# Kernel tuning notes

Hardware: AMD Instinct MI355X
Metric: run time of the kernel (lower is better)

Reference implementation:

```python
import jax, jax.numpy as jnp
import numpy as np

B, N, F = 32, 1024, 32
EPS = 1e-5


def _bn(h):
    # torch BatchNorm1d(x.size(1)) applied to [B, N, C]: normalizes each node index
    # over (batch, channel) axes, training mode, biased variance, weight=1, bias=0.
    m = h.mean(axis=(0, 2), keepdims=True)
    v = h.var(axis=(0, 2), keepdims=True)
    return (h - m) / jnp.sqrt(v + EPS)


def setup_inputs() -> dict:
    key = jax.random.key(0)
    ks = jax.random.split(key, 16)
    x = jax.random.normal(ks[0], (B, N, F), dtype=jnp.float32)
    adj = jax.random.uniform(ks[1], (B, N, N), dtype=jnp.float32)

    def w(k, i, o):
        return jax.random.normal(k, (i, o), dtype=jnp.float32) * (1.0 / np.sqrt(i))

    inp = {
        'x': x, 'adj': adj,
        'W1': w(ks[2], F, 4), 'b1': jnp.zeros((4,), jnp.float32),
        'W2': w(ks[3], 4, 2), 'b2': jnp.zeros((2,), jnp.float32),
        'W3': w(ks[4], 6, 4), 'b3': jnp.zeros((4,), jnp.float32),
        'W5': w(ks[5], 6, 4), 'b5': jnp.zeros((4,), jnp.float32),
        'W7': w(ks[6], 6, 4), 'b7': jnp.zeros((4,), jnp.float32),
        'Wl': w(ks[7], 24, 3), 'bl': jnp.zeros((3,), jnp.float32),
    }
    return inp


def reference(x, adj, W1, b1, W2, b2, W3, b3, W5, b5, W7, b7, Wl, bl):
    n = adj.shape[-1]
    # DenseGCNConv normalization (identical for every conv call): set diag to 1,
    # then D^{-1/2} A D^{-1/2} with degree clamped at 1. Precompute once.
    diag = jnp.eye(n, dtype=bool)
    A = jnp.where(diag, jnp.asarray(1.0, adj.dtype), adj)  # [B,N,N]
    d = jnp.clip(A.sum(-1), 1.0, None) ** -0.5              # [B,N]
    A = d[:, :, None] * A * d[:, None, :]

    def gcn(h, W, b):
        return jnp.matmul(A, jnp.matmul(h, W)) + b

    def block(h, Wa, ba):
        x1 = _bn(jax.nn.relu(gcn(h, Wa, ba)))      # [B,N,4]
        x2 = _bn(jax.nn.relu(gcn(x1, W2, b2)))     # [B,N,2] (conv2 reused)
        x12 = jnp.concatenate([x1, x2], axis=-1)   # [B,N,6]
        return x12, x12.max(axis=1)                # pooled [B,6]

    h, p1 = block(x, W1, b1)
    h, p2 = block(h, W3, b3)
    h, p3 = block(h, W5, b5)
    h, p4 = block(h, W7, b7)
    out = jnp.concatenate([p1, p2, p3, p4], axis=-1)  # [B,24]
    ypred = out @ Wl + bl                             # [B,3]
    return ypred
```

## Files before the change

### kernel.cpp

```cpp
#include <hip/hip_runtime.h>
#include <hip/hip_fp16.h>

#define NB 32
#define NN 1024

typedef _Float16 h2 __attribute__((ext_vector_type(2)));
typedef _Float16 h8 __attribute__((ext_vector_type(8)));

static const size_t F_D     = 0;
static const size_t F_STATS = 32768;
static const size_t F_XW1   = 49152;
static constexpr size_t F_Y[8] = {180224, 311296, 376832, 507904,
                                  573440, 704512, 770048, 901120};
static const size_t AH_BYTE_OFF  = 3866624;
static const size_t WS_NEED_HALF = AH_BYTE_OFF + (size_t)NB*NN*NN*2;

__device__ __forceinline__ float fdot2f(h2 a, h2 b, float c) {
#if __has_builtin(__builtin_amdgcn_fdot2)
    return __builtin_amdgcn_fdot2(a, b, c, false);
#else
    return c + (float)a[0]*(float)b[0] + (float)a[1]*(float)b[1];
#endif
}

__global__ __launch_bounds__(256)
void k0_prep(const float* __restrict__ adj, const float* __restrict__ x,
             const float* __restrict__ W1, float* __restrict__ dd,
             float* __restrict__ xw1, float* __restrict__ stats,
             __half* __restrict__ ahw)
{
    const int tid = threadIdx.x;
    const int bx  = blockIdx.x;
    if (bx < 8192) {
        const int lane = tid & 63, wid = tid >> 6;
        const int row = bx * 4 + wid;
        const int n = row & (NN - 1);
        const float4* arow = (const float4*)(adj + (size_t)row * NN);
        uint2* hrow = (uint2*)(ahw + (size_t)row * NN);
        float s = 0.f;
        #pragma unroll
        for (int it = 0; it < 4; ++it) {
            const int idx = lane + it * 64;
            float4 v = arow[idx];
            const int k0 = idx * 4;
            v.x = (k0 + 0 == n) ? 1.f : v.x;
            v.y = (k0 + 1 == n) ? 1.f : v.y;
            v.z = (k0 + 2 == n) ? 1.f : v.z;
            v.w = (k0 + 3 == n) ? 1.f : v.w;
            s += v.x + v.y + v.z + v.w;
            if (ahw) {
                __half2 h01 = __floats2half2_rn(v.x, v.y);
                __half2 h23 = __floats2half2_rn(v.z, v.w);
                uint2 u;
                u.x = *(unsigned*)&h01; u.y = *(unsigned*)&h23;
                hrow[idx] = u;
            }
        }
        #pragma unroll
        for (int m = 1; m < 64; m <<= 1) s += __shfl_xor(s, m);
        if (lane == 0) dd[row] = rsqrtf(fmaxf(s, 1.f));
    } else if (bx < 8320) {
        const int id = (bx - 8192) * 256 + tid;
        const float4* xr = (const float4*)(x + (size_t)id * 32);
        float in[32];
        #pragma unroll
        for (int i = 0; i < 8; ++i) {
            float4 v = xr[i];
            in[4*i]=v.x; in[4*i+1]=v.y; in[4*i+2]=v.z; in[4*i+3]=v.w;
        }
        float o[4] = {0.f,0.f,0.f,0.f};
        #pragma unroll
        for (int i = 0; i < 32; ++i)
            #pragma unroll
            for (int c = 0; c < 4; ++c) o[c] += in[i] * W1[i*4+c];
        *(float4*)(xw1 + (size_t)id * 4) = make_float4(o[0],o[1],o[2],o[3]);
    } else {
        const int id = (bx - 8320) * 256 + tid;
        stats[id] = 0.f;
    }
}

template<int CIN1, int CIN2, int COUT>
__global__ __launch_bounds__(512, 4)
void pass_half(const __half* __restrict__ ah, const float* __restrict__ dd,
               const float* __restrict__ xw1,
               const float* __restrict__ src1, const float* __restrict__ st1,
               const float* __restrict__ src2, const float* __restrict__ st2,
               const float* __restrict__ W, const float* __restrict__ bias,
               float* __restrict__ Y, float* __restrict__ stout)
{
    constexpr int HG = 8*COUT + 4;
    __shared__ _Float16 XPt[128 * HG];
    const int tid = threadIdx.x, lane = tid & 63, wid = tid >> 6;
    const int g = lane >> 5, l32 = lane & 31;
    const int b = blockIdx.x >> 4;
    const int tile = (blockIdx.x & 15) << 6;

    for (int k = tid; k < NN; k += 512) {
        float xw[COUT];
        if constexpr (CIN1 == 0) {
            const float4 v = *(const float4*)(xw1 + ((size_t)b*NN + k) * 4);
            xw[0]=v.x; xw[1]=v.y; xw[2]=v.z; xw[3]=v.w;
        } else {
            float in[CIN1 + CIN2];
            {
                const float cnt = 1.f / (32.f * CIN1);
                const float m  = st1[k] * cnt;
                const float ms = st1[NN + k] * cnt;
                const float iv = rsqrtf(ms - m*m + 1e-5f);
                const float4 v = *(const float4*)(src1 + ((size_t)b*NN + k) * CIN1);
                in[0]=(v.x-m)*iv; in[1]=(v.y-m)*iv; in[2]=(v.z-m)*iv; in[3]=(v.w-m)*iv;
            }
            if constexpr (CIN2 > 0) {
                const float cnt = 1.f / (32.f * CIN2);
                const float m  = st2[k] * cnt;
                const float ms = st2[NN + k] * cnt;
                const float iv = rsqrtf(ms - m*m + 1e-5f);
                const float2 v = *(const float2*)(src2 + ((size_t)b*NN + k) * CIN2);
                in[CIN1+0]=(v.x-m)*iv; in[CIN1+1]=(v.y-m)*iv;
            }
            #pragma unroll
            for (int c = 0; c < COUT; ++c) {
                float s = 0.f;
                #pragma unroll
                for (int i = 0; i < CIN1+CIN2; ++i) s += in[i]*W[i*COUT+c];
                xw[c] = s;
            }
        }
        const float dk = dd[b*NN + k];
        const int mbase = (k>>3)*HG + ((k>>1)&3)*(2*COUT) + (k&1);
        #pragma unroll
        for (int c = 0; c < COUT; ++c)
            XPt[mbase + 2*c] = (_Float16)(xw[c]*dk);
    }
    __syncthreads();

    const int r0 = tile + wid*8 + g*4;
    const __half* ab[4];
    #pragma unroll
    for (int j = 0; j < 4; ++j)
        ab[j] = ah + ((size_t)(b*NN + r0 + j)) * NN;

    float acc[4][COUT];
    #pragma unroll
    for (int j = 0; j < 4; ++j)
        #pragma unroll
        for (int c = 0; c < COUT; ++c) acc[j][c] = 0.f;

    #pragma unroll
    for (int it = 0; it < 4; ++it) {
        const int k = it*256 + l32*8;
        h8 av[4];
        #pragma unroll
        for (int j = 0; j < 4; ++j) av[j] = *(const h8*)(ab[j] + k);
        const h8* xp = (const h8*)&XPt[(k>>3) * HG];
        h8 xt[COUT];
        #pragma unroll
        for (int q = 0; q < COUT; ++q) xt[q] = xp[q];
        const h2* x2 = (const h2*)&xt[0];
        #pragma unroll
        for (int j = 0; j < 4; ++j) {
            const h2* a2 = (const h2*)&av[j];
            #pragma unroll
            for (int c = 0; c < COUT; ++c) {
                float s = acc[j][c];
                #pragma unroll
                for (int p = 0; p < 4; ++p)
                    s = fdot2f(a2[p], x2[p*COUT + c], s);
                acc[j][c] = s;
            }
        }
    }

    #pragma unroll
    for (int j = 0; j < 4; ++j)
        #pragma unroll
        for (int c = 0; c < COUT; ++c) {
            float v = acc[j][c];
            v += __shfl_xor(v, 1);  v += __shfl_xor(v, 2);
            v += __shfl_xor(v, 4);  v += __shfl_xor(v, 8);
            v += __shfl_xor(v, 16);
            acc[j][c] = v;
        }
    if (l32 == 0) {
        #pragma unroll
        for (int j = 0; j < 4; ++j) {
            const int n = r0 + j;
            const float dn = dd[b*NN + n];
            float s = 0.f, q2 = 0.f;
            float y[COUT];
            #pragma unroll
            for (int c = 0; c < COUT; ++c) {
                float t = acc[j][c] * dn + bias[c];
                t = fmaxf(t, 0.f);
                y[c] = t; s += t; q2 += t*t;
            }
            if constexpr (COUT == 4)
                *(float4*)(Y + ((size_t)(b*NN + n))*4) = make_float4(y[0],y[1],y[2],y[3]);
            else
                *(float2*)(Y + ((size_t)(b*NN + n))*2) = make_float2(y[0],y[1]);
            atomicAdd(stout + n, s);
            atomicAdd(stout + NN + n, q2);
        }
    }
}

template<int CIN1, int CIN2, int COUT>
__global__ __launch_bounds__(512)
void pass_f32(const float* __restrict__ adj, const float* __restrict__ dd,
              const float* __restrict__ xw1,
              const float* __restrict__ src1, const float* __restrict__ st1,
              const float* __restrict__ src2, const float* __restrict__ st2,
              const float* __restrict__ W, const float* __restrict__ bias,
              float* __restrict__ Y, float* __restrict__ stout)
{
    __shared__ float XP[COUT][NN + (NN/32)*4];
    const int tid  = threadIdx.x;
    const int b    = blockIdx.x >> 5;
    const int tile = (blockIdx.x & 31) * 32;

    for (int k = tid; k < NN; k += 512) {
        float xw[COUT];
        if constexpr (CIN1 == 0) {
            const float4 v = *(const float4*)(xw1 + ((size_t)b*NN + k) * 4);
            xw[0]=v.x; xw[1]=v.y; xw[2]=v.z; xw[3]=v.w;
        } else {
            float in[CIN1 + CIN2];
            {
                const float cnt = 1.f / (32.f * CIN1);
                float m  = st1[k] * cnt;
                float ms = st1[NN + k] * cnt;
                float iv = rsqrtf(ms - m*m + 1e-5f);
                const float4 v = *(const float4*)(src1 + ((size_t)b*NN + k) * CIN1);
                in[0]=(v.x-m)*iv; in[1]=(v.y-m)*iv; in[2]=(v.z-m)*iv; in[3]=(v.w-m)*iv;
            }
            if constexpr (CIN2 > 0) {
                const float cnt = 1.f / (32.f * CIN2);
                float m  = st2[k] * cnt;
                float ms = st2[NN + k] * cnt;
                float iv = rsqrtf(ms - m*m + 1e-5f);
                const float2 v = *(const float2*)(src2 + ((size_t)b*NN + k) * CIN2);
                in[CIN1+0]=(v.x-m)*iv; in[CIN1+1]=(v.y-m)*iv;
            }
            #pragma unroll
            for (int c = 0; c < COUT; ++c) {
                float s = 0.f;
                #pragma unroll
                for (int i = 0; i < CIN1+CIN2; ++i) s += in[i]*W[i*COUT+c];
                xw[c] = s;
            }
        }
        const float dk = dd[(size_t)b*NN + k];
        const int mk = k + ((k >> 5) << 2);
        #pragma unroll
        for (int c = 0; c < COUT; ++c) XP[c][mk] = xw[c]*dk;
    }
    __syncthreads();

    const int lane = tid & 63, wid = tid >> 6;
    const int r0 = tile + wid * 4;
    float acc[4][COUT];
    #pragma unroll
    for (int j = 0; j < 4; ++j)
        #pragma unroll
        for (int c = 0; c < COUT; ++c) acc[j][c] = 0.f;
    float dn[4]; size_t rb[4];
    #pragma unroll
    for (int j = 0; j < 4; ++j) {
        dn[j] = dd[(size_t)b*NN + r0 + j];
        rb[j] = ((size_t)(b*NN + r0 + j)) * NN;
    }
    #pragma unroll
    for (int it = 0; it < 4; ++it) {
        const int kw = 4 * (lane + 64 * it);
        const int mb = kw + ((kw >> 5) << 2);
        float xwv[COUT][4];
        #pragma unroll
        for (int c = 0; c < COUT; ++c) {
            const float4 v = *(const float4*)&XP[c][mb];
            xwv[c][0]=v.x; xwv[c][1]=v.y; xwv[c][2]=v.z; xwv[c][3]=v.w;
        }
        #pragma unroll
        for (int j = 0; j < 4; ++j) {
            const int rr = r0 + j;
            float4 a = *(const float4*)(adj + rb[j] + kw);
            a.x = (kw + 0 == rr) ? 1.f : a.x;
            a.y = (kw + 1 == rr) ? 1.f : a.y;
            a.z = (kw + 2 == rr) ? 1.f : a.z;
            a.w = (kw + 3 == rr) ? 1.f : a.w;
            #pragma unroll
            for (int c = 0; c < COUT; ++c) {
                float s = acc[j][c];
                s = fmaf(a.x, xwv[c][0], s); s = fmaf(a.y, xwv[c][1], s);
                s = fmaf(a.z, xwv[c][2], s); s = fmaf(a.w, xwv[c][3], s);
                acc[j][c] = s;
            }
        }
    }
    #pragma unroll
    for (int j = 0; j < 4; ++j) {
        #pragma unroll
        for (int c = 0; c < COUT; ++c) {
            float v = acc[j][c];
            #pragma unroll
            for (int m = 1; m < 64; m <<= 1) v += __shfl_xor(v, m);
            acc[j][c] = v;
        }
        if (lane == 0) {
            float s = 0.f, q = 0.f;
            #pragma unroll
            for (int c = 0; c < COUT; ++c) {
                float y = acc[j][c] * dn[j] + bias[c];
                y = fmaxf(y, 0.f);
                Y[((size_t)(b*NN + r0 + j)) * COUT + c] = y;
                s += y; q += y * y;
            }
            atomicAdd(stout + (r0 + j), s);
            atomicAdd(stout + NN + (r0 + j), q);
        }
    }
}

__global__ __launch_bounds__(256)
void k_final(const float* __restrict__ Y1, const float* __restrict__ Y2,
             const float* __restrict__ Y3, const float* __restrict__ Y4,
             const float* __restrict__ Y5, const float* __restrict__ Y6,
             const float* __restrict__ Y7, const float* __restrict__ Y8,
             const float* __restrict__ stats,
             const float* __restrict__ Wl, const float* __restrict__ bl,
             float* __restrict__ out)
{
    const float* Ya[4] = {Y1, Y3, Y5, Y7};
    const float* Yb[4] = {Y2, Y4, Y6, Y8};
    const int b = blockIdx.x, tid = threadIdx.x;
    float mx[24];
    #pragma unroll
    for (int i = 0; i < 24; ++i) mx[i] = -3.4e38f;

    for (int n = tid; n < NN; n += 256) {
        #pragma unroll
        for (int g = 0; g < 4; ++g) {
            {
                const float* st = stats + (size_t)(2*g) * 2048;
                const float cnt = 1.f / 128.f;
                float m  = st[n] * cnt;
                float ms = st[NN + n] * cnt;
                float iv = rsqrtf(ms - m*m + 1e-5f);
                const float4 v = *(const float4*)(Ya[g] + ((size_t)b*NN + n) * 4);
                mx[g*6+0] = fmaxf(mx[g*6+0], (v.x - m) * iv);
                mx[g*6+1] = fmaxf(mx[g*6+1], (v.y - m) * iv);
                mx[g*6+2] = fmaxf(mx[g*6+2], (v.z - m) * iv);
                mx[g*6+3] = fmaxf(mx[g*6+3], (v.w - m) * iv);
            }
            {
                const float* st = stats + (size_t)(2*g+1) * 2048;
                const float cnt = 1.f / 64.f;
                float m  = st[n] * cnt;
                float ms = st[NN + n] * cnt;
                float iv = rsqrtf(ms - m*m + 1e-5f);
                const float2 v = *(const float2*)(Yb[g] + ((size_t)b*NN + n) * 2);
                mx[g*6+4] = fmaxf(mx[g*6+4], (v.x - m) * iv);
                mx[g*6+5] = fmaxf(mx[g*6+5], (v.y - m) * iv);
            }
        }
    }
    const int lane = tid & 63, wid = tid >> 6;
    #pragma unroll
    for (int i = 0; i < 24; ++i) {
        float v = mx[i];
        #pragma unroll
        for (int m = 1; m < 64; m <<= 1) v = fmaxf(v, __shfl_xor(v, m));
        mx[i] = v;
    }
    __shared__ float red[4][24];
    __shared__ float pooled[24];
    if (lane == 0) {
        #pragma unroll
        for (int i = 0; i < 24; ++i) red[wid][i] = mx[i];
    }
    __syncthreads();
    if (tid < 24)
        pooled[tid] = fmaxf(fmaxf(red[0][tid], red[1][tid]),
                            fmaxf(red[2][tid], red[3][tid]));
    __syncthreads();
    if (tid < 3) {
        float s = bl[tid];
        #pragma unroll
        for (int c = 0; c < 24; ++c) s += pooled[c] * Wl[c*3 + tid];
        out[b*3 + tid] = s;
    }
}

extern "C" void kernel_launch(void* const* d_in, const int* in_sizes, int n_in,
                              void* d_out, int out_size, void* d_ws, size_t ws_size,
                              hipStream_t stream)
{
    const float* x   = (const float*)d_in[0];
    const float* adj = (const float*)d_in[1];
    const float* W1  = (const float*)d_in[2];
    const float* b1  = (const float*)d_in[3];
    const float* W2  = (const float*)d_in[4];
    const float* b2  = (const float*)d_in[5];
    const float* W3  = (const float*)d_in[6];
    const float* b3  = (const float*)d_in[7];
    const float* W5  = (const float*)d_in[8];
    const float* b5  = (const float*)d_in[9];
    const float* W7  = (const float*)d_in[10];
    const float* b7  = (const float*)d_in[11];
    const float* Wl  = (const float*)d_in[12];
    const float* bl  = (const float*)d_in[13];
    float* out = (float*)d_out;

    float* wsf   = (float*)d_ws;
    float* dd    = wsf + F_D;
    float* stats = wsf + F_STATS;
    float* xw1   = wsf + F_XW1;
    float* Y[8];
    #pragma unroll
    for (int i = 0; i < 8; ++i) Y[i] = wsf + F_Y[i];
    __half* ah = (__half*)((char*)d_ws + AH_BYTE_OFF);
    const bool use_half = (ws_size >= WS_NEED_HALF);

    k0_prep<<<8384, 256, 0, stream>>>(adj, x, W1, dd, xw1, stats,
                                      use_half ? ah : nullptr);

    #define STT(i) (stats + (i)*2048)
    if (use_half) {
        const dim3 pg(512), pb(512);
        pass_half<0,0,4><<<pg, pb, 0, stream>>>(ah, dd, xw1,
            nullptr, nullptr, nullptr, nullptr, nullptr, b1, Y[0], STT(0));
        pass_half<4,0,2><<<pg, pb, 0, stream>>>(ah, dd, nullptr,
            Y[0], STT(0), nullptr, nullptr, W2, b2, Y[1], STT(1));
        pass_half<4,2,4><<<pg, pb, 0, stream>>>(ah, dd, nullptr,
            Y[0], STT(0), Y[1], STT(1), W3, b3, Y[2], STT(2));
        pass_half<4,0,2><<<pg, pb, 0, stream>>>(ah, dd, nullptr,
            Y[2], STT(2), nullptr, nullptr, W2, b2, Y[3], STT(3));
        pass_half<4,2,4><<<pg, pb, 0, stream>>>(ah, dd, nullptr,
            Y[2], STT(2), Y[3], STT(3), W5, b5, Y[4], STT(4));
        pass_half<4,0,2><<<pg, pb, 0, stream>>>(ah, dd, nullptr,
            Y[4], STT(4), nullptr, nullptr, W2, b2, Y[5], STT(5));
        pass_half<4,2,4><<<pg, pb, 0, stream>>>(ah, dd, nullptr,
            Y[4], STT(4), Y[5], STT(5), W7, b7, Y[6], STT(6));
        pass_half<4,0,2><<<pg, pb, 0, stream>>>(ah, dd, nullptr,
            Y[6], STT(6), nullptr, nullptr, W2, b2, Y[7], STT(7));
    } else {
        const dim3 pg(1024), pb(512);
        pass_f32<0,0,4><<<pg, pb, 0, stream>>>(adj, dd, xw1,
            nullptr, nullptr, nullptr, nullptr, nullptr, b1, Y[0], STT(0));
        pass_f32<4,0,2><<<pg, pb, 0, stream>>>(adj, dd, nullptr,
            Y[0], STT(0), nullptr, nullptr, W2, b2, Y[1], STT(1));
        pass_f32<4,2,4><<<pg, pb, 0, stream>>>(adj, dd, nullptr,
            Y[0], STT(0), Y[1], STT(1), W3, b3, Y[2], STT(2));
        pass_f32<4,0,2><<<pg, pb, 0, stream>>>(adj, dd, nullptr,
            Y[2], STT(2), nullptr, nullptr, W2, b2, Y[3], STT(3));
        pass_f32<4,2,4><<<pg, pb, 0, stream>>>(adj, dd, nullptr,
            Y[2], STT(2), Y[3], STT(3), W5, b5, Y[4], STT(4));
        pass_f32<4,0,2><<<pg, pb, 0, stream>>>(adj, dd, nullptr,
            Y[4], STT(4), nullptr, nullptr, W2, b2, Y[5], STT(5));
        pass_f32<4,2,4><<<pg, pb, 0, stream>>>(adj, dd, nullptr,
            Y[4], STT(4), Y[5], STT(5), W7, b7, Y[6], STT(6));
        pass_f32<4,0,2><<<pg, pb, 0, stream>>>(adj, dd, nullptr,
            Y[6], STT(6), nullptr, nullptr, W2, b2, Y[7], STT(7));
    }
    #undef STT

    k_final<<<32, 256, 0, stream>>>(Y[0], Y[1], Y[2], Y[3], Y[4], Y[5], Y[6], Y[7],
                                    stats, Wl, bl, out);
}
```

Before: 182.0 us.

## Double-buffer adjacency tiles into LDS via async global_load_lds with XOR swizzle

Stages the fp16 adjacency row tile for each 256-column chunk into a double-buffered shared-memory region using direct global-to-LDS loads, so the next chunk's fetch overlaps the current chunk's dot products. The first chunk is issued before the X*W preprocessing to hide its latency, and an XOR swizzle on columns is meant to avoid LDS bank conflicts. This adds 64KB of LDS per block, which likely lowers occupancy below the launch-bounds target, and adds barriers each chunk.

```diff
diff --git a/kernel.cpp b/kernel.cpp
--- a/kernel.cpp
+++ b/kernel.cpp
@@ -80,6 +80,28 @@
     }
 }
 
+__device__ __forceinline__ void stage_chunk(const __half* __restrict__ ah,
+        int rowbase, int wid, int lane, int ck, char* sbuf)
+{
+    #pragma unroll
+    for (int i = 0; i < 4; ++i) {
+        const int ob = (wid << 12) + (i << 10);
+        const int o  = ob + (lane << 4);
+        const int row = o >> 9;
+        const int scol = (o & 511) ^ ((row & 7) << 4);
+        const char* g = (const char*)ah +
+            (((size_t)(rowbase + row)) * NN + (size_t)ck * 256) * 2 + scol;
+#if __has_builtin(__builtin_amdgcn_global_load_lds)
+        __builtin_amdgcn_global_load_lds(
+            (const __attribute__((address_space(1))) void*)g,
+            (__attribute__((address_space(3))) void*)(sbuf + ob),
+            16, 0, 0);
+#else
+        *(float4*)(sbuf + o) = *(const float4*)g;
+#endif
+    }
+}
+
 template<int CIN1, int CIN2, int COUT>
 __global__ __launch_bounds__(512, 4)
 void pass_half(const __half* __restrict__ ah, const float* __restrict__ dd,
@@ -89,12 +111,16 @@
                const float* __restrict__ W, const float* __restrict__ bias,
                float* __restrict__ Y, float* __restrict__ stout)
 {
-    constexpr int HG = 8*COUT + 4;
+    constexpr int HG = (COUT == 4) ? 40 : 24;
+    __shared__ char sA[2][32768];
     __shared__ _Float16 XPt[128 * HG];
     const int tid = threadIdx.x, lane = tid & 63, wid = tid >> 6;
     const int g = lane >> 5, l32 = lane & 31;
     const int b = blockIdx.x >> 4;
     const int tile = (blockIdx.x & 15) << 6;
+    const int rowbase = b * NN + tile;
+
+    stage_chunk(ah, rowbase, wid, lane, 0, sA[0]);
 
     for (int k = tid; k < NN; k += 512) {
         float xw[COUT];
@@ -133,34 +159,35 @@
         for (int c = 0; c < COUT; ++c)
             XPt[mbase + 2*c] = (_Float16)(xw[c]*dk);
     }
+    asm volatile("s_waitcnt vmcnt(0)" ::: "memory");
     __syncthreads();
 
-    const int r0 = tile + wid*8 + g*4;
-    const __half* ab[4];
+    const int tr0 = wid*8 + g*4;
+    float acc[4][COUT];
     #pragma unroll
     for (int j = 0; j < 4; ++j)
-        ab[j] = ah + ((size_t)(b*NN + r0 + j)) * NN;
-
-    float acc[4][COUT];
-    #pragma unroll
-    for (int j = 0; j < 4; ++j)
         #pragma unroll
         for (int c = 0; c < COUT; ++c) acc[j][c] = 0.f;
 
-    #pragma unroll
-    for (int it = 0; it < 4; ++it) {
-        const int k = it*256 + l32*8;
-        h8 av[4];
-        #pragma unroll
-        for (int j = 0; j < 4; ++j) av[j] = *(const h8*)(ab[j] + k);
-        const h8* xp = (const h8*)&XPt[(k>>3) * HG];
+    int buf = 0;
+    for (int ck = 0; ck < 4; ++ck) {
+        if (ck < 3) stage_chunk(ah, rowbase, wid, lane, ck+1, sA[buf^1]);
+
+        const int g_i = ck*32 + l32;
         h8 xt[COUT];
-        #pragma unroll
-        for (int q = 0; q < COUT; ++q) xt[q] = xp[q];
+        {
+            const h8* xp = (const h8*)&XPt[g_i * HG];
+            #pragma unroll
+            for (int q = 0; q < COUT; ++q) xt[q] = xp[q];
+        }
         const h2* x2 = (const h2*)&xt[0];
+
         #pragma unroll
         for (int j = 0; j < 4; ++j) {
-            const h2* a2 = (const h2*)&av[j];
+            const int tr = tr0 + j;
+            const h8 av = *(const h8*)(&sA[buf][(tr << 9) +
+                                      ((l32 ^ (tr & 7)) << 4)]);
+            const h2* a2 = (const h2*)&av;
             #pragma unroll
             for (int c = 0; c < COUT; ++c) {
                 float s = acc[j][c];
@@ -170,6 +197,9 @@
                 acc[j][c] = s;
             }
         }
+        asm volatile("s_waitcnt vmcnt(0)" ::: "memory");
+        __syncthreads();
+        buf ^= 1;
     }
 
     #pragma unroll
@@ -185,7 +215,7 @@
     if (l32 == 0) {
         #pragma unroll
         for (int j = 0; j < 4; ++j) {
-            const int n = r0 + j;
+            const int n = tile + tr0 + j;
             const float dn = dd[b*NN + n];
             float s = 0.f, q2 = 0.f;
             float y[COUT];
```

Measured after the change: 206.2 us. +13.3%, slower.

## Stage adjacency tiles into LDS via async global_load_lds overlapping XW compute

Applied to the files above, without the earlier changes.

Each block now handles 32 rows instead of 64 and issues asynchronous global-to-LDS loads (global_load_lds) for its 64KB slab of the half-precision adjacency before computing the scaled XW vector. This lets the adjacency fetch overlap the preamble work. The XW operand layout changes to a channel-major array, the wave reduction now spans 64 lanes, and the grid doubles while occupancy bounds drop to 2 blocks per CU. The cost is heavier LDS use (64KB plus XW per block), lower occupancy, and the preamble being recomputed twice as often across blocks. There is also some risk in the hand-written vmcnt waits and the fallback path.

```diff
diff --git a/kernel.cpp b/kernel.cpp
--- a/kernel.cpp
+++ b/kernel.cpp
@@ -80,8 +80,27 @@
     }
 }
 
+__device__ __forceinline__ void stage_chunk32(const __half* __restrict__ ah,
+        int rowbase, int wid, int lane, int ck, char* sbase)
+{
+    #pragma unroll
+    for (int i = 0; i < 4; ++i) {
+        char* dst = sbase + (ck << 15) + (wid << 12) + (i << 10);
+        const char* g = (const char*)ah +
+            (((size_t)(rowbase + (wid << 2) + i)) << 11) + (ck << 10) + (lane << 4);
+#if __has_builtin(__builtin_amdgcn_global_load_lds)
+        __builtin_amdgcn_global_load_lds(
+            (const __attribute__((address_space(1))) void*)g,
+            (__attribute__((address_space(3))) void*)dst,
+            16, 0, 0);
+#else
+        *(float4*)(dst + lane * 16) = *(const float4*)g;
+#endif
+    }
+}
+
 template<int CIN1, int CIN2, int COUT>
-__global__ __launch_bounds__(512, 4)
+__global__ __launch_bounds__(512, 2)
 void pass_half(const __half* __restrict__ ah, const float* __restrict__ dd,
                const float* __restrict__ xw1,
                const float* __restrict__ src1, const float* __restrict__ st1,
@@ -89,14 +108,19 @@
                const float* __restrict__ W, const float* __restrict__ bias,
                float* __restrict__ Y, float* __restrict__ stout)
 {
-    constexpr int HG = 8*COUT + 4;
-    __shared__ _Float16 XPt[128 * HG];
+    __shared__ char sA[65536];
+    __shared__ _Float16 XPc[COUT][NN];
     const int tid = threadIdx.x, lane = tid & 63, wid = tid >> 6;
-    const int g = lane >> 5, l32 = lane & 31;
-    const int b = blockIdx.x >> 4;
-    const int tile = (blockIdx.x & 15) << 6;
-
-    for (int k = tid; k < NN; k += 512) {
+    const int b = blockIdx.x >> 5;
+    const int tile = (blockIdx.x & 31) << 5;
+    const int rowbase = b * NN + tile;
+
+    stage_chunk32(ah, rowbase, wid, lane, 0, sA);
+    stage_chunk32(ah, rowbase, wid, lane, 1, sA);
+
+    #pragma unroll
+    for (int kk = 0; kk < 2; ++kk) {
+        const int k = tid + kk * 512;
         float xw[COUT];
         if constexpr (CIN1 == 0) {
             const float4 v = *(const float4*)(xw1 + ((size_t)b*NN + k) * 4);
@@ -128,45 +152,40 @@
             }
         }
         const float dk = dd[b*NN + k];
-        const int mbase = (k>>3)*HG + ((k>>1)&3)*(2*COUT) + (k&1);
         #pragma unroll
         for (int c = 0; c < COUT; ++c)
-            XPt[mbase + 2*c] = (_Float16)(xw[c]*dk);
-    }
-    __syncthreads();
-
-    const int r0 = tile + wid*8 + g*4;
-    const __half* ab[4];
+            XPc[c][k] = (_Float16)(xw[c]*dk);
+    }
+
+    asm volatile("s_waitcnt lgkmcnt(0)" ::: "memory");
+    __builtin_amdgcn_s_barrier();
+
+    float acc[4][COUT];
     #pragma unroll
     for (int j = 0; j < 4; ++j)
-        ab[j] = ah + ((size_t)(b*NN + r0 + j)) * NN;
-
-    float acc[4][COUT];
-    #pragma unroll
-    for (int j = 0; j < 4; ++j)
         #pragma unroll
         for (int c = 0; c < COUT; ++c) acc[j][c] = 0.f;
 
     #pragma unroll
-    for (int it = 0; it < 4; ++it) {
-        const int k = it*256 + l32*8;
-        h8 av[4];
-        #pragma unroll
-        for (int j = 0; j < 4; ++j) av[j] = *(const h8*)(ab[j] + k);
-        const h8* xp = (const h8*)&XPt[(k>>3) * HG];
+    for (int ck = 0; ck < 2; ++ck) {
+        if (ck == 0) asm volatile("s_waitcnt vmcnt(4)" ::: "memory");
+        else         asm volatile("s_waitcnt vmcnt(0)" ::: "memory");
         h8 xt[COUT];
         #pragma unroll
-        for (int q = 0; q < COUT; ++q) xt[q] = xp[q];
-        const h2* x2 = (const h2*)&xt[0];
+        for (int c = 0; c < COUT; ++c)
+            xt[c] = *(const h8*)&XPc[c][(ck << 9) + (lane << 3)];
         #pragma unroll
         for (int j = 0; j < 4; ++j) {
-            const h2* a2 = (const h2*)&av[j];
-            #pragma unroll
-            for (int c = 0; c < COUT; ++c) {
+            const h8 av = *(const h8*)(sA + (ck << 15) + (wid << 12) +
+                                       (j << 10) + (lane << 4));
+            const h2* a2 = (const h2*)&av;
+            #pragma unroll
+            for (int c = 0; c < COUT; ++c) {
+                const h2* x2 = (const h2*)&xt[c];
                 float s = acc[j][c];
                 #pragma unroll
                 for (int p = 0; p < 4; ++p)
-                    s = fdot2f(a2[p], x2[p*COUT + c], s);
+                    s = fdot2f(a2[p], x2[p], s);
                 acc[j][c] = s;
             }
         }
@@ -179,13 +198,13 @@
             float v = acc[j][c];
             v += __shfl_xor(v, 1);  v += __shfl_xor(v, 2);
             v += __shfl_xor(v, 4);  v += __shfl_xor(v, 8);
-            v += __shfl_xor(v, 16);
+            v += __shfl_xor(v, 16); v += __shfl_xor(v, 32);
             acc[j][c] = v;
         }
-    if (l32 == 0) {
+    if (lane == 0) {
         #pragma unroll
         for (int j = 0; j < 4; ++j) {
-            const int n = r0 + j;
+            const int n = tile + (wid << 2) + j;
             const float dn = dd[b*NN + n];
             float s = 0.f, q2 = 0.f;
             float y[COUT];
@@ -426,7 +445,7 @@
 
     #define STT(i) (stats + (i)*2048)
     if (use_half) {
-        const dim3 pg(512), pb(512);
+        const dim3 pg(1024), pb(512);
         pass_half<0,0,4><<<pg, pb, 0, stream>>>(ah, dd, xw1,
             nullptr, nullptr, nullptr, nullptr, nullptr, b1, Y[0], STT(0));
         pass_half<4,0,2><<<pg, pb, 0, stream>>>(ah, dd, nullptr,
```

Result: slower. 230.1 us (+26.4%).
